# Kernel tuning notes

Hardware: AMD Instinct MI355X
Metric: run time of the kernel (lower is better)

The kernel has to match this reference:

```python
import jax, jax.numpy as jnp
import numpy as np

DIM = 512   # model dim C (num_heads=1 -> head_dim = C)
NK = 128    # tokens per key-batch element
BQ = 512    # query batch
BK = 256    # key batch
NC = 1000   # num_classes for visual_fc head


def _ln(x, g, b, eps=1e-5):
    m = x.mean(-1, keepdims=True)
    v = x.var(-1, keepdims=True)
    return (x - m) * jax.lax.rsqrt(v + eps) * g + b


def _l2norm(x, eps=1e-12):  # F.normalize(p=2, dim=-1)
    n = jnp.linalg.norm(x, axis=-1, keepdims=True)
    return x / jnp.maximum(n, eps)


def setup_inputs() -> dict:
    key = jax.random.key(0)
    ks = jax.random.split(key, 8)
    s = 0.02
    return {
        "qx": jax.random.normal(ks[0], (BQ, 1, DIM), dtype=jnp.float32),
        "kx": jax.random.normal(ks[1], (BK, NK, DIM), dtype=jnp.float32),
        "key_padding_mask": jax.random.randint(ks[2], (BK, NK), 0, 2).astype(bool),
        "logit_scale": jnp.array([np.log(100.0)], dtype=jnp.float32),
        "g_q": jnp.ones((DIM,), jnp.float32), "b_q": jnp.zeros((DIM,), jnp.float32),
        "g_k": jnp.ones((DIM,), jnp.float32), "b_k": jnp.zeros((DIM,), jnp.float32),
        "wq": jax.random.normal(ks[3], (DIM, DIM), dtype=jnp.float32) * s,
        "wk": jax.random.normal(ks[4], (DIM, DIM), dtype=jnp.float32) * s,
        "w1": jax.random.normal(ks[5], (4 * DIM, DIM), dtype=jnp.float32) * s,
        "b1": jnp.zeros((4 * DIM,), jnp.float32),
        "w2": jax.random.normal(ks[6], (NC, 4 * DIM), dtype=jnp.float32) * s,
        "b2": jnp.zeros((NC,), jnp.float32),
    }


def reference(qx, kx, key_padding_mask, logit_scale,
              g_q, b_q, g_k, b_k, wq, wk, w1, b1, w2, b2):
    C = qx.shape[-1]
    scale = C ** -0.5  # num_heads=1 so head_dim == C
    # cross-batch single-query attention (Attention.forward)
    q = _ln(qx, g_q, b_q) @ wq.T                       # [Bq,1,C]
    k = _ln(kx, g_k, b_k) @ wk.T                       # [Bk,Nk,C]
    attn = jnp.einsum('qoc,knc->qkn', q, k) * scale    # [Bq,Bk,Nk]
    attn = jnp.where(key_padding_mask[None, :, :], -jnp.inf, attn)
    attn = jax.nn.softmax(attn, axis=-1)
    v = jnp.einsum('knc,qkn->qkc', kx, attn)           # [Bq,Bk,C]
    # two_branch head
    h = jax.nn.relu(qx[:, 0, :] @ w1.T + b1)           # [Bq,4C]
    x1 = h @ w2.T + b2                                 # [Bq,NC]
    x2 = jnp.einsum('qkc,qoc->qk', _l2norm(v), _l2norm(qx)) * jnp.exp(logit_scale)[0]
    return (x1, x2)
```

## Files before the change

### kernel.cpp

```cpp
#include <hip/hip_runtime.h>

typedef unsigned short u16;
typedef unsigned int u32;
typedef short bf16x8s __attribute__((ext_vector_type(8)));
typedef float f32x4 __attribute__((ext_vector_type(4)));

#define SCALE_C 0.044194173824159216f
#define MFMA16 __builtin_amdgcn_mfma_f32_16x16x32_bf16

__device__ __forceinline__ u16 f2bf(float f){
  union { float f; u32 u; } c; c.f = f;
  u32 u = c.u;
  return (u16)((u + 0x7fffu + ((u >> 16) & 1u)) >> 16);
}

__device__ __forceinline__ void gload16(const void* g, void* l){
  __builtin_amdgcn_global_load_lds((const __attribute__((address_space(1))) void*)g,
                                   (__attribute__((address_space(3))) void*)l, 16, 0, 0);
}

#define OFF_KXB  ((size_t)0)
#define OFF_G    (OFF_KXB + 33554432)
#define OFF_W2B  (OFF_G + 8388608)
#define OFF_H    (OFF_W2B + 4096000)
#define OFF_W1B  (OFF_H + 2097152)
#define OFF_QLN  (OFF_W1B + 2097152)
#define OFF_QHAT (OFF_QLN + 524288)
#define OFF_QXB  (OFF_QHAT + 524288)
#define OFF_P    (OFF_QXB + 524288)
#define OFF_M2   (OFF_P + 524288)
#define OFF_WQB  (OFF_M2 + 524288)
#define OFF_WCT  (OFF_WQB + 524288)
#define OFF_KM   (OFF_WCT + 524288)
#define OFF_KR   (OFF_KM + 131072)
#define OFF_T2   (OFF_KR + 131072)
#define OFF_FLAG (OFF_T2 + 4096)

__global__ __launch_bounds__(512) void k_phase1(
    const float* __restrict__ qx, const float* __restrict__ kx,
    const int* __restrict__ maskw,
    const float* __restrict__ g_q, const float* __restrict__ b_q,
    const float* __restrict__ wq, const float* __restrict__ wk,
    const float* __restrict__ w1, const float* __restrict__ b1,
    const float* __restrict__ w2, const float* __restrict__ b2,
    u16* __restrict__ kxb, float* __restrict__ km, float* __restrict__ kr,
    u16* __restrict__ Gm,
    u16* __restrict__ qln, u16* __restrict__ qhat,
    u16* __restrict__ wct, u16* __restrict__ w2b, u16* __restrict__ hbuf,
    float* __restrict__ t2s, int* __restrict__ flag, float* __restrict__ x1o)
{
  __shared__ __align__(16) u16 lBig[16384];
  __shared__ float redq[8][2];
  __shared__ int smax;
  const int bid = blockIdx.x, tid = threadIdx.x;
  const int lane = tid & 63, w = tid >> 6;
  const int l15 = lane & 15, lg = lane >> 4;

  if (bid < 256){
    u16* lk = lBig;
    const int z = bid;
    const int a0 = (w>>2)*64, b0 = (w&3)*32;
    float s[16] = {0,0,0,0,0,0,0,0,0,0,0,0,0,0,0,0};
    float sq[16] = {0,0,0,0,0,0,0,0,0,0,0,0,0,0,0,0};
    f32x4 acc[4][2] = {};
    for (int ch = 0; ch < 4; ch++){
      #pragma unroll
      for (int i = 0; i < 16; i++){
        int r = w*16 + i;
        float2 v = *(const float2*)(kx + ((size_t)z*128 + r)*512 + ch*128 + lane*2);
        s[i] += v.x + v.y; sq[i] += v.x*v.x + v.y*v.y;
        u32 pk = f2bf(v.x) | ((u32)f2bf(v.y)<<16);
        *(u32*)(kxb + ((size_t)z*128 + r)*512 + ch*128 + lane*2) = pk;
        *(u32*)&lk[r*128 + ((lane*2) ^ ((r&7)<<3))] = pk;
      }
      __syncthreads();
      #pragma unroll
      for (int kk = 0; kk < 4; kk++){
        int cgr = kk*4 + lg;
        bf16x8s a[4], b[2];
        #pragma unroll
        for (int i2 = 0; i2 < 4; i2++){
          int r = a0 + i2*16 + l15;
          a[i2] = *(const bf16x8s*)&lk[r*128 + ((cgr*8) ^ ((r&7)<<3))];
        }
        #pragma unroll
        for (int j = 0; j < 2; j++){
          int r = b0 + j*16 + l15;
          b[j] = *(const bf16x8s*)&lk[r*128 + ((cgr*8) ^ ((r&7)<<3))];
        }
        #pragma unroll
        for (int i2 = 0; i2 < 4; i2++)
          #pragma unroll
          for (int j = 0; j < 2; j++)
            acc[i2][j] = MFMA16(a[i2], b[j], acc[i2][j], 0,0,0);
      }
      __syncthreads();
    }
    #pragma unroll
    for (int i = 0; i < 16; i++){
      float ss = s[i], qq = sq[i];
      #pragma unroll
      for (int o = 1; o < 64; o <<= 1){ ss += __shfl_xor(ss,o); qq += __shfl_xor(qq,o); }
      if (lane == 0){
        int r = w*16 + i;
        float mean = ss*(1.0f/512.0f);
        float var  = qq*(1.0f/512.0f) - mean*mean;
        km[z*128+r] = mean; kr[z*128+r] = rsqrtf(var + 1e-5f);
      }
    }
    u16* G = Gm + (size_t)z*16384;
    #pragma unroll
    for (int i2 = 0; i2 < 4; i2++)
      #pragma unroll
      for (int j = 0; j < 2; j++)
        #pragma unroll
        for (int r = 0; r < 4; r++)
          G[(size_t)(a0 + i2*16 + lg*4 + r)*128 + b0 + j*16 + l15] = f2bf(acc[i2][j][r]);
  } else if (bid < 512){
    const int row = (bid-256)*2 + (tid>>8);
    const int t = tid & 255;
    float2 v = *(const float2*)(qx + (size_t)row*512 + t*2);
    float s = v.x+v.y, sq = v.x*v.x+v.y*v.y;
    #pragma unroll
    for (int o = 1; o < 64; o <<= 1){ s += __shfl_xor(s,o); sq += __shfl_xor(sq,o); }
    if (lane == 0){ redq[w][0]=s; redq[w][1]=sq; }
    __syncthreads();
    const int h4 = (tid>>8)*4;
    s  = redq[h4][0]+redq[h4+1][0]+redq[h4+2][0]+redq[h4+3][0];
    sq = redq[h4][1]+redq[h4+1][1]+redq[h4+2][1]+redq[h4+3][1];
    float mean = s*(1.0f/512.0f);
    float var  = sq*(1.0f/512.0f) - mean*mean;
    float rstd = rsqrtf(var + 1e-5f);
    float il2  = 1.0f / fmaxf(sqrtf(sq), 1e-12f);
    float2 g  = *(const float2*)(g_q + t*2);
    float2 bb = *(const float2*)(b_q + t*2);
    u32 a  = f2bf((v.x-mean)*rstd*g.x+bb.x) | ((u32)f2bf((v.y-mean)*rstd*g.y+bb.y)<<16);
    u32 hh = f2bf(v.x*il2) | ((u32)f2bf(v.y*il2)<<16);
    *(u32*)(qln  + (size_t)row*512 + t*2) = a;
    *(u32*)(qhat + (size_t)row*512 + t*2) = hh;
  } else if (bid < 1512){
    int i = (bid-512)*512 + tid;
    float4 v = *(const float4*)(w2 + (size_t)i*4);
    uint2 p;
    p.x = f2bf(v.x)|((u32)f2bf(v.y)<<16); p.y = f2bf(v.z)|((u32)f2bf(v.w)<<16);
    *(uint2*)(w2b + (size_t)i*4) = p;
  } else if (bid < 1640){
    const int t = bid - 1512;
    const int m0 = (t >> 4)*64, n0 = (t & 15)*128;
    const int w4 = w & 3;
    const int nb = (w >> 2)*64;
    const int wr = (w4>>1)*32, wc = (w4&1)*32;
    u16* shA = lBig;
    u16* shB = lBig + 4096;
    f32x4 acc[2][2] = {};
    for (int kc = 0; kc < 512; kc += 64){
      {
        int row = tid >> 3, c8 = (tid & 7)*8;
        float4 a0 = *(const float4*)(qx + (size_t)(m0+row)*512 + kc + c8);
        float4 a1 = *(const float4*)(qx + (size_t)(m0+row)*512 + kc + c8 + 4);
        u16 ta[8] = {f2bf(a0.x),f2bf(a0.y),f2bf(a0.z),f2bf(a0.w),
                     f2bf(a1.x),f2bf(a1.y),f2bf(a1.z),f2bf(a1.w)};
        *(uint4*)&shA[row*64 + (((tid&7) ^ (row&7))*8)] = *(uint4*)ta;
        #pragma unroll
        for (int s2 = 0; s2 < 2; s2++){
          int u = tid + s2*512;
          int rowb = u >> 3, cb8 = (u & 7)*8;
          float4 b0 = *(const float4*)(w1 + (size_t)(n0+rowb)*512 + kc + cb8);
          float4 b1v = *(const float4*)(w1 + (size_t)(n0+rowb)*512 + kc + cb8 + 4);
          u16 tb[8] = {f2bf(b0.x),f2bf(b0.y),f2bf(b0.z),f2bf(b0.w),
                       f2bf(b1v.x),f2bf(b1v.y),f2bf(b1v.z),f2bf(b1v.w)};
          *(uint4*)&shB[rowb*64 + (((u&7) ^ (rowb&7))*8)] = *(uint4*)tb;
        }
      }
      __syncthreads();
      #pragma unroll
      for (int kk = 0; kk < 2; kk++){
        int cgr = kk*4 + lg;
        int ra0 = wr + l15, ra1 = wr + 16 + l15;
        int rb0 = nb + wc + l15, rb1 = nb + wc + 16 + l15;
        bf16x8s a0 = *(const bf16x8s*)&shA[ra0*64 + ((cgr ^ (ra0&7))*8)];
        bf16x8s a1 = *(const bf16x8s*)&shA[ra1*64 + ((cgr ^ (ra1&7))*8)];
        bf16x8s b0 = *(const bf16x8s*)&shB[rb0*64 + ((cgr ^ (rb0&7))*8)];
        bf16x8s b1 = *(const bf16x8s*)&shB[rb1*64 + ((cgr ^ (rb1&7))*8)];
        acc[0][0]=MFMA16(a0,b0,acc[0][0],0,0,0);
        acc[0][1]=MFMA16(a0,b1,acc[0][1],0,0,0);
        acc[1][0]=MFMA16(a1,b0,acc[1][0],0,0,0);
        acc[1][1]=MFMA16(a1,b1,acc[1][1],0,0,0);
      }
      __syncthreads();
    }
    #pragma unroll
    for (int i = 0; i < 2; i++)
      #pragma unroll
      for (int j = 0; j < 2; j++){
        int col = n0 + nb + wc + j*16 + l15;
        float bv = b1[col];
        #pragma unroll
        for (int r = 0; r < 4; r++){
          int row = m0 + wr + i*16 + lg*4 + r;
          hbuf[(size_t)row*2048 + col] = f2bf(fmaxf(acc[i][j][r] + bv, 0.0f));
        }
      }
  } else if (bid < 1704){
    const int t = bid - 1640;
    const int f0 = (t>>3)*64, c0 = (t&7)*64;
    const int w4 = w & 3;
    const int wr = (w4>>1)*32, wc = (w4&1)*32;
    u16* shA = lBig;
    u16* shB = lBig + 4096;
    f32x4 acc[2][2] = {};
    for (int i0 = 0; i0 < 512; i0 += 64){
      const int ii = tid >> 3;
      const int cc8 = (tid & 7) * 8;
      float4 va0 = *(const float4*)(wk + (size_t)(i0+ii)*512 + f0 + cc8);
      float4 va1 = *(const float4*)(wk + (size_t)(i0+ii)*512 + f0 + cc8 + 4);
      float4 vb0 = *(const float4*)(wq + (size_t)(i0+ii)*512 + c0 + cc8);
      float4 vb1 = *(const float4*)(wq + (size_t)(i0+ii)*512 + c0 + cc8 + 4);
      #pragma unroll
      for (int e = 0; e < 8; e++){
        float fa = e < 4 ? (&va0.x)[e] : (&va1.x)[e-4];
        float fb = e < 4 ? (&vb0.x)[e] : (&vb1.x)[e-4];
        int rowc = cc8 + e;
        int idx = rowc*64 + (((ii>>3) ^ (rowc&7))*8 + (ii&7));
        shA[idx] = f2bf(fa);
        shB[idx] = f2bf(fb);
      }
      __syncthreads();
      #pragma unroll
      for (int kk = 0; kk < 2; kk++){
        int cgr = kk*4 + lg;
        int ra0 = wr + l15, ra1 = wr + 16 + l15;
        int rb0 = wc + l15, rb1 = wc + 16 + l15;
        bf16x8s a0 = *(const bf16x8s*)&shA[ra0*64 + ((cgr ^ (ra0&7))*8)];
        bf16x8s a1 = *(const bf16x8s*)&shA[ra1*64 + ((cgr ^ (ra1&7))*8)];
        bf16x8s b0 = *(const bf16x8s*)&shB[rb0*64 + ((cgr ^ (rb0&7))*8)];
        bf16x8s b1 = *(const bf16x8s*)&shB[rb1*64 + ((cgr ^ (rb1&7))*8)];
        acc[0][0]=MFMA16(a0,b0,acc[0][0],0,0,0);
        acc[0][1]=MFMA16(a0,b1,acc[0][1],0,0,0);
        acc[1][0]=MFMA16(a1,b0,acc[1][0],0,0,0);
        acc[1][1]=MFMA16(a1,b1,acc[1][1],0,0,0);
      }
      __syncthreads();
    }
    if (tid < 256){
      #pragma unroll
      for (int i = 0; i < 2; i++)
        #pragma unroll
        for (int j = 0; j < 2; j++)
          #pragma unroll
          for (int r = 0; r < 4; r++)
            wct[(size_t)(f0 + wr + i*16 + lg*4 + r)*512 + c0 + wc + j*16 + l15]
                = f2bf(acc[i][j][r]);
    }
  } else if (bid < 1954){
    int i = (bid-1704)*2048 + tid*4;
    #pragma unroll
    for (int e = 0; e < 4; e++){
      int idx = i + e;
      x1o[idx] = b2[idx % 1000];
    }
  } else {
    if (tid == 0) smax = 0;
    t2s[tid] = 0.0f;
    __syncthreads();
    int mx = 0;
    for (int i = tid; i < 8192; i += 512){ int v = maskw[i]; mx = v > mx ? v : mx; }
    #pragma unroll
    for (int o = 1; o < 64; o <<= 1){ int t2 = __shfl_xor(mx,o); mx = t2 > mx ? t2 : mx; }
    if ((tid & 63) == 0) atomicMax(&smax, mx);
    __syncthreads();
    if (tid == 0) *flag = (smax <= 1) ? 1 : 0;
  }
}

__device__ __forceinline__ void gemm_body(const u16* __restrict__ Ap, const u16* __restrict__ Bp,
    int M, int N, int K, int m0, int n0, int tid,
    u16 (*lA)[64], u16 (*lB)[64], f32x4 (&acc)[2][2])
{
  const int lane = tid & 63, w = tid >> 6;
  const int wr = (w >> 1)*32, wc = (w & 1)*32;
  const int l15 = lane & 15, lg = lane >> 4;
  for (int kc = 0; kc < K; kc += 64){
    #pragma unroll
    for (int s = 0; s < 2; s++){
      int u = tid + s*256;
      int row = u >> 3, cg = u & 7;
      int sw = (cg ^ (row & 7)) * 8;
      uint4 va = make_uint4(0,0,0,0);
      if (m0 + row < M) va = *(const uint4*)(Ap + (size_t)(m0+row)*K + kc + cg*8);
      *(uint4*)&lA[row][sw] = va;
      uint4 vb = make_uint4(0,0,0,0);
      if (n0 + row < N) vb = *(const uint4*)(Bp + (size_t)(n0+row)*K + kc + cg*8);
      *(uint4*)&lB[row][sw] = vb;
    }
    __syncthreads();
    #pragma unroll
    for (int kk = 0; kk < 2; kk++){
      int cgr = kk*4 + lg;
      int ra0 = wr + l15, ra1 = wr + 16 + l15;
      int rb0 = wc + l15, rb1 = wc + 16 + l15;
      bf16x8s a0 = *(const bf16x8s*)&lA[ra0][(cgr ^ (ra0&7))*8];
      bf16x8s a1 = *(const bf16x8s*)&lA[ra1][(cgr ^ (ra1&7))*8];
      bf16x8s b0 = *(const bf16x8s*)&lB[rb0][(cgr ^ (rb0&7))*8];
      bf16x8s b1 = *(const bf16x8s*)&lB[rb1][(cgr ^ (rb1&7))*8];
      acc[0][0] = MFMA16(a0,b0,acc[0][0],0,0,0);
      acc[0][1] = MFMA16(a0,b1,acc[0][1],0,0,0);
      acc[1][0] = MFMA16(a1,b0,acc[1][0],0,0,0);
      acc[1][1] = MFMA16(a1,b1,acc[1][1],0,0,0);
    }
    __syncthreads();
  }
}

__global__ __launch_bounds__(256) void k_phase2(
    const u16* __restrict__ qln, const u16* __restrict__ wct,
    const float* __restrict__ g_k, u16* __restrict__ m2, float* __restrict__ t2s,
    const u16* __restrict__ hbuf, const u16* __restrict__ w2b,
    float* __restrict__ x1o)
{
  __shared__ __align__(16) u16 lA[64][64], lB[64][64];
  f32x4 acc[2][2] = {};
  const int bid = blockIdx.x, tid = threadIdx.x;
  const int lane = tid & 63, w = tid >> 6;
  const int wr = (w >> 1)*32, wc = (w & 1)*32;
  const int l15 = lane & 15, lg = lane >> 4;
  if (bid < 512){
    const int ks = bid >> 7;
    const int t  = bid & 127;
    const int m0 = (t >> 4)*64, n0 = (t & 15)*64;
    for (int kc = ks*512; kc < ks*512 + 512; kc += 64){
      #pragma unroll
      for (int s = 0; s < 2; s++){
        int u = tid + s*256;
        int row = u >> 3, cg = u & 7;
        int sw = (cg ^ (row & 7)) * 8;
        *(uint4*)&lA[row][sw] = *(const uint4*)(hbuf + (size_t)(m0+row)*2048 + kc + cg*8);
        uint4 vb = make_uint4(0,0,0,0);
        if (n0 + row < 1000) vb = *(const uint4*)(w2b + (size_t)(n0+row)*2048 + kc + cg*8);
        *(uint4*)&lB[row][sw] = vb;
      }
      __syncthreads();
      #pragma unroll
      for (int kk = 0; kk < 2; kk++){
        int cgr = kk*4 + lg;
        int ra0 = wr + l15, ra1 = wr + 16 + l15;
        int rb0 = wc + l15, rb1 = wc + 16 + l15;
        bf16x8s a0 = *(const bf16x8s*)&lA[ra0][(cgr ^ (ra0&7))*8];
        bf16x8s a1 = *(const bf16x8s*)&lA[ra1][(cgr ^ (ra1&7))*8];
        bf16x8s b0 = *(const bf16x8s*)&lB[rb0][(cgr ^ (rb0&7))*8];
        bf16x8s b1 = *(const bf16x8s*)&lB[rb1][(cgr ^ (rb1&7))*8];
        acc[0][0]=MFMA16(a0,b0,acc[0][0],0,0,0);
        acc[0][1]=MFMA16(a0,b1,acc[0][1],0,0,0);
        acc[1][0]=MFMA16(a1,b0,acc[1][0],0,0,0);
        acc[1][1]=MFMA16(a1,b1,acc[1][1],0,0,0);
      }
      __syncthreads();
    }
    #pragma unroll
    for (int i = 0; i < 2; i++)
      #pragma unroll
      for (int j = 0; j < 2; j++){
        int col = n0 + wc + j*16 + l15;
        if (col < 1000){
          #pragma unroll
          for (int r = 0; r < 4; r++){
            int row = m0 + wr + i*16 + lg*4 + r;
            atomicAdd(&x1o[(size_t)row*1000 + col], acc[i][j][r]);
          }
        }
      }
  } else {
    const int b = bid - 512;
    int m0 = (b>>3)*64, n0 = (b&7)*64;
    gemm_body(qln, wct, 512,512,512, m0,n0, tid, lA, lB, acc);
    #pragma unroll
    for (int i = 0; i < 2; i++){
      #pragma unroll
      for (int r = 0; r < 4; r++){
        int row = m0 + wr + i*16 + lg*4 + r;
        float part = 0.f;
        #pragma unroll
        for (int j = 0; j < 2; j++){
          int col = n0 + wc + j*16 + l15;
          float e = SCALE_C * acc[i][j][r] * g_k[col];
          m2[(size_t)row*512 + col] = f2bf(e);
          part += e;
        }
        #pragma unroll
        for (int o = 1; o < 16; o <<= 1) part += __shfl_xor(part, o);
        if (l15 == 0) atomicAdd(&t2s[row], part);
      }
    }
  }
}

__global__ __launch_bounds__(512, 4) void k_attn(
    const u16* __restrict__ kxb, const u16* __restrict__ Gm,
    const u16* __restrict__ m2, const u16* __restrict__ qhat,
    const float* __restrict__ km, const float* __restrict__ kr,
    const float* __restrict__ t2s, const void* __restrict__ maskp,
    const int* __restrict__ flagp, const float* __restrict__ lsp,
    float* __restrict__ x2)
{
  __shared__ __align__(16) u16 sb[24576];
  __shared__ float lt2[128];
  __shared__ float lNum[128][2], lDen[128][2];
  u16* lP = sb;

  const int bid = blockIdx.x;
  const int kb = (bid & 7)*32 + ((bid >> 3) & 31);
  const int q0 = (bid >> 8) * 128;
  const int tid = threadIdx.x, lane = tid & 63, w = tid >> 6;
  const int wr = (w >> 1)*32, wcol = (w & 1)*64;
  const int l15 = lane & 15, lg = lane >> 4;
  const int fl = *flagp;
  const float expls = __expf(lsp[0]);

  if (tid < 128) lt2[tid] = t2s[q0 + tid];

  float kmv[4], krv[4], mbv[4];
  #pragma unroll
  for (int j = 0; j < 4; j++){
    int gn = kb*128 + wcol + j*16 + l15;
    kmv[j] = km[gn]; krv[j] = kr[gn];
    int mv = fl ? ((const int*)maskp)[gn] : (int)((const unsigned char*)maskp)[gn];
    mbv[j] = mv ? -1e30f : 0.0f;
  }

  const u16* KX = kxb + (size_t)kb * 65536;
  f32x4 aS[2][4] = {}, aD[2][4] = {};

  const int srow  = w*16 + (lane >> 2);
  const int sslot = (lane & 3) ^ ((srow >> 1) & 3);
  const int lofs  = w*512;

  #define STAGE(p) do{                                                         \
    const int kc_ = (p)*32;                                                    \
    u16* b_ = sb + ((p)&1)*12288;                                              \
    gload16(KX   + (size_t)srow*512      + kc_ + sslot*8, b_ + lofs);          \
    gload16(m2   + (size_t)(q0+srow)*512 + kc_ + sslot*8, b_ + 4096 + lofs);   \
    gload16(qhat + (size_t)(q0+srow)*512 + kc_ + sslot*8, b_ + 8192 + lofs);   \
  }while(0)

  STAGE(0);
  #pragma unroll
  for (int p = 0; p < 16; p++){
    if (p < 15){
      STAGE(p+1);
      asm volatile("s_waitcnt vmcnt(3)" ::: "memory");
    } else {
      asm volatile("s_waitcnt vmcnt(0)" ::: "memory");
    }
    __builtin_amdgcn_s_barrier();
    __builtin_amdgcn_sched_barrier(0);
    const u16* lb  = sb + (p&1)*12288;
    const u16* lKX = lb;
    const u16* lM2 = lb + 4096;
    const u16* lQH = lb + 8192;
    const int rA0 = wr + l15, rA1 = wr + 16 + l15;
    bf16x8s am0 = *(const bf16x8s*)&lM2[rA0*32 + ((lg ^ ((rA0>>1)&3))*8)];
    bf16x8s am1 = *(const bf16x8s*)&lM2[rA1*32 + ((lg ^ ((rA1>>1)&3))*8)];
    bf16x8s aq0 = *(const bf16x8s*)&lQH[rA0*32 + ((lg ^ ((rA0>>1)&3))*8)];
    bf16x8s aq1 = *(const bf16x8s*)&lQH[rA1*32 + ((lg ^ ((rA1>>1)&3))*8)];
    __builtin_amdgcn_s_setprio(1);
    #pragma unroll
    for (int j = 0; j < 4; j++){
      int rB = wcol + j*16 + l15;
      bf16x8s bk = *(const bf16x8s*)&lKX[rB*32 + ((lg ^ ((rB>>1)&3))*8)];
      aS[0][j] = MFMA16(am0, bk, aS[0][j], 0,0,0);
      aS[1][j] = MFMA16(am1, bk, aS[1][j], 0,0,0);
      aD[0][j] = MFMA16(aq0, bk, aD[0][j], 0,0,0);
      aD[1][j] = MFMA16(aq1, bk, aD[1][j], 0,0,0);
    }
    __builtin_amdgcn_s_setprio(0);
    __builtin_amdgcn_sched_barrier(0);
    __builtin_amdgcn_s_barrier();
  }
  __syncthreads();

  #pragma unroll
  for (int i = 0; i < 2; i++){
    #pragma unroll
    for (int r = 0; r < 4; r++){
      int rowl = wr + i*16 + lg*4 + r;
      float t2v = lt2[rowl];
      float sn = 0.f;
      #pragma unroll
      for (int j = 0; j < 4; j++){
        float L = krv[j]*(aS[i][j][r] - kmv[j]*t2v) + mbv[j];
        float e = __expf(L);
        aS[i][j][r] = e;
        sn += e * aD[i][j][r];
      }
      #pragma unroll
      for (int o = 1; o < 16; o <<= 1) sn += __shfl_xor(sn, o);
      if (l15 == 0) lNum[rowl][w&1] = sn;
      #pragma unroll
      for (int j = 0; j < 4; j++){
        int n = wcol + j*16 + l15;
        lP[rowl*128 + ((n>>3)^(rowl&7))*8 + (n&7)] = f2bf(aS[i][j][r]);
      }
    }
  }
  __syncthreads();

  f32x4 aT[2][4] = {};
  const u16* Gk = Gm + (size_t)kb * 16384;
  #pragma unroll
  for (int kk = 0; kk < 4; kk++){
    int cgr = kk*4 + lg;
    int rA0 = wr + l15, rA1 = wr + 16 + l15;
    bf16x8s p0 = *(const bf16x8s*)&lP[rA0*128 + ((cgr^(rA0&7))*8)];
    bf16x8s p1 = *(const bf16x8s*)&lP[rA1*128 + ((cgr^(rA1&7))*8)];
    #pragma unroll
    for (int j = 0; j < 4; j++){
      int mcol = wcol + j*16 + l15;
      bf16x8s bg = *(const bf16x8s*)(Gk + (size_t)mcol*128 + kk*32 + lg*8);
      aT[0][j] = MFMA16(p0, bg, aT[0][j], 0,0,0);
      aT[1][j] = MFMA16(p1, bg, aT[1][j], 0,0,0);
    }
  }
  #pragma unroll
  for (int i = 0; i < 2; i++){
    #pragma unroll
    for (int r = 0; r < 4; r++){
      int rowl = wr + i*16 + lg*4 + r;
      float sd = 0.f;
      #pragma unroll
      for (int j = 0; j < 4; j++) sd += aT[i][j][r] * aS[i][j][r];
      #pragma unroll
      for (int o = 1; o < 16; o <<= 1) sd += __shfl_xor(sd, o);
      if (l15 == 0) lDen[rowl][w&1] = sd;
    }
  }
  __syncthreads();

  if (tid < 128){
    float num  = lNum[tid][0] + lNum[tid][1];
    float den2 = lDen[tid][0] + lDen[tid][1];
    float den  = fmaxf(sqrtf(fmaxf(den2, 0.0f)), 1e-12f);
    x2[(size_t)(q0 + tid)*256 + kb] = expls * num / den;
  }
}

extern "C" void kernel_launch(void* const* d_in, const int* in_sizes, int n_in,
                              void* d_out, int out_size, void* d_ws, size_t ws_size,
                              hipStream_t stream)
{
  (void)in_sizes; (void)n_in; (void)out_size; (void)ws_size;
  const float* qx  = (const float*)d_in[0];
  const float* kx  = (const float*)d_in[1];
  const void*  mask= d_in[2];
  const float* lsp = (const float*)d_in[3];
  const float* g_q = (const float*)d_in[4];
  const float* b_q = (const float*)d_in[5];
  const float* g_k = (const float*)d_in[6];
  const float* wq  = (const float*)d_in[8];
  const float* wk  = (const float*)d_in[9];
  const float* w1  = (const float*)d_in[10];
  const float* b1  = (const float*)d_in[11];
  const float* w2  = (const float*)d_in[12];
  const float* b2  = (const float*)d_in[13];

  char* ws = (char*)d_ws;
  u16* kxb  = (u16*)(ws + OFF_KXB);
  u16* Gm   = (u16*)(ws + OFF_G);
  u16* w2b  = (u16*)(ws + OFF_W2B);
  u16* hbuf = (u16*)(ws + OFF_H);
  u16* qln  = (u16*)(ws + OFF_QLN);
  u16* qhat = (u16*)(ws + OFF_QHAT);
  u16* m2   = (u16*)(ws + OFF_M2);
  u16* wct  = (u16*)(ws + OFF_WCT);
  float* km  = (float*)(ws + OFF_KM);
  float* kr  = (float*)(ws + OFF_KR);
  float* t2s = (float*)(ws + OFF_T2);
  int*   flag= (int*)(ws + OFF_FLAG);
  float* x1o = (float*)d_out;
  float* x2o = (float*)d_out + 512*1000;

  k_phase1<<<dim3(1955), dim3(512), 0, stream>>>(
      qx, kx, (const int*)mask, g_q, b_q, wq, wk, w1, b1, w2, b2,
      kxb, km, kr, Gm, qln, qhat, wct, w2b, hbuf, t2s, flag, x1o);
  k_phase2<<<dim3(576), dim3(256), 0, stream>>>(
      qln, wct, g_k, m2, t2s, hbuf, w2b, x1o);
  k_attn<<<dim3(1024), dim3(512), 0, stream>>>(
      kxb, Gm, m2, qhat, km, kr, t2s, mask, flag, lsp, x2o);
}
```

Baseline: 119.9 us.

## Move x1 head GEMM from phase2 into the tail of the attention kernel

```diff
diff --git a/kernel.cpp b/kernel.cpp
--- a/kernel.cpp
+++ b/kernel.cpp
@@ -273,25 +273,25 @@
   }
 }
 
-__device__ __forceinline__ void gemm_body(const u16* __restrict__ Ap, const u16* __restrict__ Bp,
-    int M, int N, int K, int m0, int n0, int tid,
-    u16 (*lA)[64], u16 (*lB)[64], f32x4 (&acc)[2][2])
+__global__ __launch_bounds__(256) void k_phase2(
+    const u16* __restrict__ qln, const u16* __restrict__ wct,
+    const float* __restrict__ g_k, u16* __restrict__ m2, float* __restrict__ t2s)
 {
+  __shared__ __align__(16) u16 lA[64][64], lB[64][64];
+  f32x4 acc[2][2] = {};
+  const int bid = blockIdx.x, tid = threadIdx.x;
   const int lane = tid & 63, w = tid >> 6;
   const int wr = (w >> 1)*32, wc = (w & 1)*32;
   const int l15 = lane & 15, lg = lane >> 4;
-  for (int kc = 0; kc < K; kc += 64){
+  const int m0 = (bid>>3)*64, n0 = (bid&7)*64;
+  for (int kc = 0; kc < 512; kc += 64){
     #pragma unroll
     for (int s = 0; s < 2; s++){
       int u = tid + s*256;
       int row = u >> 3, cg = u & 7;
       int sw = (cg ^ (row & 7)) * 8;
-      uint4 va = make_uint4(0,0,0,0);
-      if (m0 + row < M) va = *(const uint4*)(Ap + (size_t)(m0+row)*K + kc + cg*8);
-      *(uint4*)&lA[row][sw] = va;
-      uint4 vb = make_uint4(0,0,0,0);
-      if (n0 + row < N) vb = *(const uint4*)(Bp + (size_t)(n0+row)*K + kc + cg*8);
-      *(uint4*)&lB[row][sw] = vb;
+      *(uint4*)&lA[row][sw] = *(const uint4*)(qln + (size_t)(m0+row)*512 + kc + cg*8);
+      *(uint4*)&lB[row][sw] = *(const uint4*)(wct + (size_t)(n0+row)*512 + kc + cg*8);
     }
     __syncthreads();
     #pragma unroll
@@ -310,86 +310,22 @@
     }
     __syncthreads();
   }
-}
-
-__global__ __launch_bounds__(256) void k_phase2(
-    const u16* __restrict__ qln, const u16* __restrict__ wct,
-    const float* __restrict__ g_k, u16* __restrict__ m2, float* __restrict__ t2s,
-    const u16* __restrict__ hbuf, const u16* __restrict__ w2b,
-    float* __restrict__ x1o)
-{
-  __shared__ __align__(16) u16 lA[64][64], lB[64][64];
-  f32x4 acc[2][2] = {};
-  const int bid = blockIdx.x, tid = threadIdx.x;
-  const int lane = tid & 63, w = tid >> 6;
-  const int wr = (w >> 1)*32, wc = (w & 1)*32;
-  const int l15 = lane & 15, lg = lane >> 4;
-  if (bid < 512){
-    const int ks = bid >> 7;
-    const int t  = bid & 127;
-    const int m0 = (t >> 4)*64, n0 = (t & 15)*64;
-    for (int kc = ks*512; kc < ks*512 + 512; kc += 64){
-      #pragma unroll
-      for (int s = 0; s < 2; s++){
-        int u = tid + s*256;
-        int row = u >> 3, cg = u & 7;
-        int sw = (cg ^ (row & 7)) * 8;
-        *(uint4*)&lA[row][sw] = *(const uint4*)(hbuf + (size_t)(m0+row)*2048 + kc + cg*8);
-        uint4 vb = make_uint4(0,0,0,0);
-        if (n0 + row < 1000) vb = *(const uint4*)(w2b + (size_t)(n0+row)*2048 + kc + cg*8);
-        *(uint4*)&lB[row][sw] = vb;
-      }
-      __syncthreads();
-      #pragma unroll
-      for (int kk = 0; kk < 2; kk++){
-        int cgr = kk*4 + lg;
-        int ra0 = wr + l15, ra1 = wr + 16 + l15;
-        int rb0 = wc + l15, rb1 = wc + 16 + l15;
-        bf16x8s a0 = *(const bf16x8s*)&lA[ra0][(cgr ^ (ra0&7))*8];
-        bf16x8s a1 = *(const bf16x8s*)&lA[ra1][(cgr ^ (ra1&7))*8];
-        bf16x8s b0 = *(const bf16x8s*)&lB[rb0][(cgr ^ (rb0&7))*8];
-        bf16x8s b1 = *(const bf16x8s*)&lB[rb1][(cgr ^ (rb1&7))*8];
-        acc[0][0]=MFMA16(a0,b0,acc[0][0],0,0,0);
-        acc[0][1]=MFMA16(a0,b1,acc[0][1],0,0,0);
-        acc[1][0]=MFMA16(a1,b0,acc[1][0],0,0,0);
-        acc[1][1]=MFMA16(a1,b1,acc[1][1],0,0,0);
-      }
-      __syncthreads();
-    }
-    #pragma unroll
-    for (int i = 0; i < 2; i++)
+  #pragma unroll
+  for (int i = 0; i < 2; i++){
+    #pragma unroll
+    for (int r = 0; r < 4; r++){
+      int row = m0 + wr + i*16 + lg*4 + r;
+      float part = 0.f;
       #pragma unroll
       for (int j = 0; j < 2; j++){
         int col = n0 + wc + j*16 + l15;
-        if (col < 1000){
-          #pragma unroll
-          for (int r = 0; r < 4; r++){
-            int row = m0 + wr + i*16 + lg*4 + r;
-            atomicAdd(&x1o[(size_t)row*1000 + col], acc[i][j][r]);
-          }
-        }
-      }
-  } else {
-    const int b = bid - 512;
-    int m0 = (b>>3)*64, n0 = (b&7)*64;
-    gemm_body(qln, wct, 512,512,512, m0,n0, tid, lA, lB, acc);
-    #pragma unroll
-    for (int i = 0; i < 2; i++){
-      #pragma unroll
-      for (int r = 0; r < 4; r++){
-        int row = m0 + wr + i*16 + lg*4 + r;
-        float part = 0.f;
-        #pragma unroll
-        for (int j = 0; j < 2; j++){
-          int col = n0 + wc + j*16 + l15;
-          float e = SCALE_C * acc[i][j][r] * g_k[col];
-          m2[(size_t)row*512 + col] = f2bf(e);
-          part += e;
-        }
-        #pragma unroll
-        for (int o = 1; o < 16; o <<= 1) part += __shfl_xor(part, o);
-        if (l15 == 0) atomicAdd(&t2s[row], part);
-      }
+        float e = SCALE_C * acc[i][j][r] * g_k[col];
+        m2[(size_t)row*512 + col] = f2bf(e);
+        part += e;
+      }
+      #pragma unroll
+      for (int o = 1; o < 16; o <<= 1) part += __shfl_xor(part, o);
+      if (l15 == 0) atomicAdd(&t2s[row], part);
     }
   }
 }
@@ -400,7 +336,9 @@
     const float* __restrict__ km, const float* __restrict__ kr,
     const float* __restrict__ t2s, const void* __restrict__ maskp,
     const int* __restrict__ flagp, const float* __restrict__ lsp,
-    float* __restrict__ x2)
+    float* __restrict__ x2,
+    const u16* __restrict__ hbuf, const u16* __restrict__ w2b,
+    float* __restrict__ x1o)
 {
   __shared__ __align__(16) u16 sb[24576];
   __shared__ float lt2[128];
@@ -540,6 +478,63 @@
     float den2 = lDen[tid][0] + lDen[tid][1];
     float den  = fmaxf(sqrtf(fmaxf(den2, 0.0f)), 1e-12f);
     x2[(size_t)(q0 + tid)*256 + kb] = expls * num / den;
+  }
+
+  {
+    const int t = bid & 127, s8 = bid >> 7;
+    const int m0x = (t >> 4)*64, n0x = (t & 15)*64;
+    const int g = w >> 2;
+    const int w4 = w & 3;
+    const int wrx = (w4 >> 1)*32, wcx = (w4 & 1)*32;
+    u16* lAx = sb + g*8192;
+    u16* lBx = lAx + 4096;
+    const int tl = tid & 255;
+    f32x4 accx[2][2] = {};
+    #pragma unroll
+    for (int ch = 0; ch < 2; ch++){
+      const int kc = s8*256 + g*128 + ch*64;
+      #pragma unroll
+      for (int s2 = 0; s2 < 2; s2++){
+        int u = tl + s2*256;
+        int row = u >> 3, cg2 = u & 7;
+        int sw = (cg2 ^ (row & 7))*8;
+        *(uint4*)&lAx[row*64 + sw] =
+            *(const uint4*)(hbuf + (size_t)(m0x+row)*2048 + kc + cg2*8);
+        uint4 vb = make_uint4(0,0,0,0);
+        if (n0x + row < 1000)
+          vb = *(const uint4*)(w2b + (size_t)(n0x+row)*2048 + kc + cg2*8);
+        *(uint4*)&lBx[row*64 + sw] = vb;
+      }
+      __syncthreads();
+      #pragma unroll
+      for (int kk = 0; kk < 2; kk++){
+        int cgr = kk*4 + lg;
+        int ra0 = wrx + l15, ra1 = wrx + 16 + l15;
+        int rb0 = wcx + l15, rb1 = wcx + 16 + l15;
+        bf16x8s a0 = *(const bf16x8s*)&lAx[ra0*64 + ((cgr ^ (ra0&7))*8)];
+        bf16x8s a1 = *(const bf16x8s*)&lAx[ra1*64 + ((cgr ^ (ra1&7))*8)];
+        bf16x8s b0 = *(const bf16x8s*)&lBx[rb0*64 + ((cgr ^ (rb0&7))*8)];
+        bf16x8s b1 = *(const bf16x8s*)&lBx[rb1*64 + ((cgr ^ (rb1&7))*8)];
+        accx[0][0]=MFMA16(a0,b0,accx[0][0],0,0,0);
+        accx[0][1]=MFMA16(a0,b1,accx[0][1],0,0,0);
+        accx[1][0]=MFMA16(a1,b0,accx[1][0],0,0,0);
+        accx[1][1]=MFMA16(a1,b1,accx[1][1],0,0,0);
+      }
+      __syncthreads();
+    }
+    #pragma unroll
+    for (int i = 0; i < 2; i++)
+      #pragma unroll
+      for (int j = 0; j < 2; j++){
+        int col = n0x + wcx + j*16 + l15;
+        if (col < 1000){
+          #pragma unroll
+          for (int r = 0; r < 4; r++){
+            int row = m0x + wrx + i*16 + lg*4 + r;
+            atomicAdd(&x1o[(size_t)row*1000 + col], accx[i][j][r]);
+          }
+        }
+      }
   }
 }
 
@@ -581,8 +576,9 @@
   k_phase1<<<dim3(1955), dim3(512), 0, stream>>>(
       qx, kx, (const int*)mask, g_q, b_q, wq, wk, w1, b1, w2, b2,
       kxb, km, kr, Gm, qln, qhat, wct, w2b, hbuf, t2s, flag, x1o);
-  k_phase2<<<dim3(576), dim3(256), 0, stream>>>(
-      qln, wct, g_k, m2, t2s, hbuf, w2b, x1o);
+  k_phase2<<<dim3(64), dim3(256), 0, stream>>>(
+      qln, wct, g_k, m2, t2s);
   k_attn<<<dim3(1024), dim3(512), 0, stream>>>(
-      kxb, Gm, m2, qhat, km, kr, t2s, mask, flag, lsp, x2o);
+      kxb, Gm, m2, qhat, km, kr, t2s, mask, flag, lsp, x2o,
+      hbuf, w2b, x1o);
 }
```

Result: slower. 137.2 us (+14.4%).
